# Optimization experiments

Measured on AMD Instinct MI355X. Metric: run time of the kernel, lower is better.

Reference implementation:

```python
import jax, jax.numpy as jnp
import numpy as np

B, N, DIM, HEADS = 8, 4096, 512, 8
BASE = 10000.0


def rope_cos_sin(n, dim, base=BASE):
    k_max = dim // 2
    theta = 1.0 / base ** (jnp.arange(k_max, dtype=jnp.float32) / k_max)
    angles = jnp.arange(n, dtype=jnp.float32)[:, None] * theta  # (n, k_max)
    return jnp.cos(angles), jnp.sin(angles)


def apply_rope(x, cos, sin):
    # x: (b, n, dim); complex pairs are interleaved (even=real, odd=imag)
    xr = x[..., 0::2]
    xi = x[..., 1::2]
    out_r = cos * xr - sin * xi
    out_i = sin * xr + cos * xi
    return jnp.stack([out_r, out_i], axis=-1).reshape(x.shape)


def setup_inputs() -> dict:
    key = jax.random.key(0)
    ks = jax.random.split(key, 8)
    s = 0.02
    return {
        'x': jax.random.normal(ks[0], (B, N, DIM), jnp.float32),
        'y': jax.random.normal(ks[1], (B, N, DIM), jnp.float32),
        'Wq': jax.random.normal(ks[2], (DIM, DIM), jnp.float32) * s,
        'bq': jax.random.normal(ks[3], (DIM,), jnp.float32) * s,
        'Wk': jax.random.normal(ks[4], (DIM, DIM), jnp.float32) * s,
        'bk': jax.random.normal(ks[5], (DIM,), jnp.float32) * s,
        'lepe_w': jax.random.normal(ks[6], (DIM, 1, 3), jnp.float32) * s,
        'lepe_b': jax.random.normal(ks[7], (DIM,), jnp.float32) * s,
    }


def reference(x, y, Wq, bq, Wk, bk, lepe_w, lepe_b):
    b, n, c = x.shape
    h = HEADS
    d = c // h
    q = jax.nn.elu(x @ Wq.T + bq) + 1.0
    k = jax.nn.elu(y @ Wk.T + bk) + 1.0
    cos, sin = rope_cos_sin(n, c)
    q_rope = apply_rope(q, cos, sin).reshape(b, n, h, d).transpose(0, 2, 1, 3)
    k_rope = apply_rope(k, cos, sin).reshape(b, n, h, d).transpose(0, 2, 1, 3)
    qh = q.reshape(b, n, h, d).transpose(0, 2, 1, 3)
    kh = k.reshape(b, n, h, d).transpose(0, 2, 1, 3)
    v = y.reshape(b, n, h, d).transpose(0, 2, 1, 3)
    kmean = kh.mean(axis=2, keepdims=True)  # (b,h,1,d)
    z = 1.0 / (jnp.einsum('bhnd,bhmd->bhnm', qh, kmean) + 1e-6)  # (b,h,n,1)
    scale = n ** (-0.5)
    kv = jnp.einsum('bhnd,bhne->bhde', k_rope * scale, v * scale)  # (b,h,d,d)
    out = jnp.einsum('bhnd,bhde->bhne', q_rope, kv) * z  # (b,h,n,d)
    out = out.transpose(0, 2, 1, 3).reshape(b, n, c)
    # LePE: depthwise conv1d over value stream
    vc = v.transpose(0, 2, 1, 3).reshape(b, n, c).transpose(0, 2, 1)  # (b,c,n)
    lepe = jax.lax.conv_general_dilated(
        vc, lepe_w, window_strides=(1,), padding=[(1, 1)],
        dimension_numbers=('NCH', 'OIH', 'NCH'), feature_group_count=c)
    lepe = lepe + lepe_b[None, :, None]
    return out + lepe.transpose(0, 2, 1)
```

## Files before the change

### kernel.cpp

```cpp
#include <hip/hip_runtime.h>

#define B_ 8
#define N_ 4096
#define C_ 512
#define H_ 8

typedef _Float16 h8  __attribute__((ext_vector_type(8)));
typedef _Float16 h4v __attribute__((ext_vector_type(4)));
typedef float    f4  __attribute__((ext_vector_type(4)));

static const size_t OFF_COS  = 0;
static const size_t OFF_SIN  = (size_t)4*1024*1024;
static const size_t OFF_KRH  = (size_t)8*1024*1024;
static const size_t OFF_YH   = (size_t)40*1024*1024;
static const size_t OFF_WQH  = (size_t)72*1024*1024;
static const size_t OFF_WKH  = (size_t)72*1024*1024 + 512*1024;
static const size_t OFF_KSUM = (size_t)73*1024*1024;
static const size_t OFF_KVG  = (size_t)73*1024*1024 + 64*1024;
static const size_t OFF_KVT  = (size_t)74*1024*1024 + 64*1024;

__device__ __forceinline__ unsigned int pack2h(float a, float b){
    union { _Float16 h[2]; unsigned int u; } x;
    x.h[0] = (_Float16)a; x.h[1] = (_Float16)b; return x.u;
}

__global__ void k_tables(float* __restrict__ cosT, float* __restrict__ sinT){
    int n = blockIdx.x, j = threadIdx.x;
    double th = exp((double)j * -0.035977892078031970);
    float ang = (float)n * (float)th;
    float s, c; sincosf(ang, &s, &c);
    cosT[n*256 + j] = c; sinT[n*256 + j] = s;
}

__global__ __launch_bounds__(256) void k_prep_y(
    const float* __restrict__ y, const float* __restrict__ Wq, const float* __restrict__ Wk,
    _Float16* __restrict__ yh, _Float16* __restrict__ Wqh, _Float16* __restrict__ Wkh)
{
    int bid = blockIdx.x;
    const float* src; _Float16* dst; size_t base;
    if (bid < 8192)      { src = y;  dst = yh;  base = (size_t)bid*2048; }
    else if (bid < 8320) { src = Wq; dst = Wqh; base = (size_t)(bid-8192)*2048; }
    else                 { src = Wk; dst = Wkh; base = (size_t)(bid-8320)*2048; }
    size_t o = base + (size_t)threadIdx.x*8;
    float4 a = *(const float4*)&src[o];
    float4 b = *(const float4*)&src[o+4];
    uint4 r; r.x = pack2h(a.x,a.y); r.y = pack2h(a.z,a.w); r.z = pack2h(b.x,b.y); r.w = pack2h(b.z,b.w);
    *(uint4*)&dst[o] = r;
}

__global__ __launch_bounds__(256) void k_prep_x(const float* __restrict__ x, _Float16* __restrict__ xh){
    size_t o = (size_t)blockIdx.x*2048 + (size_t)threadIdx.x*8;
    float4 a = *(const float4*)&x[o];
    float4 b = *(const float4*)&x[o+4];
    uint4 r; r.x = pack2h(a.x,a.y); r.y = pack2h(a.z,a.w); r.z = pack2h(b.x,b.y); r.w = pack2h(b.z,b.w);
    *(uint4*)&xh[o] = r;
}

__device__ __forceinline__ void stage_tile(const _Float16* __restrict__ g, _Float16* lds, int t){
#pragma unroll
    for (int i=0;i<2;++i){
        int u = i*256 + t;
        int r = u >> 2;
        int j = (u & 3) ^ ((r ^ (r >> 2)) & 3);
        __builtin_amdgcn_global_load_lds(
            (const __attribute__((address_space(1))) void*)(g + (size_t)r*C_ + j*8),
            (__attribute__((address_space(3))) void*)(lds + (size_t)(i*256 + (t & 192))*8),
            16, 0, 0);
    }
}

template<int IS_Q>
__global__ __launch_bounds__(256, IS_Q ? 3 : 4) void k_gemm(
    const _Float16* __restrict__ A, const _Float16* __restrict__ Wh, const float* __restrict__ bias,
    const float* __restrict__ cosT, const float* __restrict__ sinT,
    _Float16* __restrict__ krh, float* __restrict__ ksum,
    const float* __restrict__ ksumIn, const _Float16* __restrict__ kvTg,
    const _Float16* __restrict__ yh, const float* __restrict__ lw, const float* __restrict__ lb,
    float* __restrict__ outp)
{
    __shared__ __align__(16) char smem[IS_Q ? 53248 : 32768];
    _Float16* qrs = (_Float16*)smem;
    _Float16* kvs = (_Float16*)(smem + 36864);

    const int t = threadIdx.x;
    const int lane = t & 63;
    const int w = t >> 6;
    const int wm = w >> 1, wn = w & 1;
    const int col0 = blockIdx.x * 128;
    const int row0 = blockIdx.y * 128;
    const int lrow = lane & 15, lg = lane >> 4;
    const int b = row0 >> 12;

    if constexpr (IS_Q){
#pragma unroll
        for (int i=0;i<4;++i){
            int idx = i*256 + t;
            int hl = idx >> 9, w9 = idx & 511, e = w9 >> 3, u8 = w9 & 7;
            int j = u8 ^ (e & 7);
            int bhh = b*H_ + (col0 >> 6) + hl;
            __builtin_amdgcn_global_load_lds(
                (const __attribute__((address_space(1))) void*)(kvTg + (size_t)bhh*4096 + e*64 + j*8),
                (__attribute__((address_space(3))) void*)(kvs + (size_t)(i*256 + (t & 192))*8),
                16, 0, 0);
        }
    }

    f4 acc[4][4] = {};
    stage_tile(A  + (size_t)row0*C_, (_Float16*)(smem), t);
    stage_tile(Wh + (size_t)col0*C_, (_Float16*)(smem + 16384), t);

    const int sw = (lrow ^ (lrow >> 2)) & 3;
    const int cK = (lg ^ sw) * 8;
    int cur = 0;

    for (int kk=0; kk<16; ++kk){
        __syncthreads();
        if (kk < 15){
            stage_tile(A  + (size_t)row0*C_ + (kk+1)*32, (_Float16*)(smem + (cur^1)*8192), t);
            stage_tile(Wh + (size_t)col0*C_ + (kk+1)*32, (_Float16*)(smem + 16384 + (cur^1)*8192), t);
        }
        const _Float16* As = (const _Float16*)(smem + cur*8192);
        const _Float16* Bs = (const _Float16*)(smem + 16384 + cur*8192);
        h8 af[4], bf[4];
#pragma unroll
        for (int mi=0; mi<4; ++mi) af[mi] = *(const h8*)&As[(wm*64 + mi*16 + lrow)*32 + cK];
#pragma unroll
        for (int ni=0; ni<4; ++ni) bf[ni] = *(const h8*)&Bs[(wn*64 + ni*16 + lrow)*32 + cK];
#pragma unroll
        for (int mi=0; mi<4; ++mi)
#pragma unroll
            for (int ni=0; ni<4; ++ni)
                acc[mi][ni] = __builtin_amdgcn_mfma_f32_16x16x32_f16(af[mi], bf[ni], acc[mi][ni], 0,0,0);
        __syncthreads();
        cur ^= 1;
    }

    const int hcol0 = col0 + wn*64;
    float bcol[4], km[4];
#pragma unroll
    for (int ni=0; ni<4; ++ni){
        int c = hcol0 + ni*16 + lrow;
        bcol[ni] = bias[c];
        km[ni] = IS_Q ? ksumIn[b*C_ + c] * (1.0f/4096.0f) : 0.0f;
    }
    float colsum[4] = {0.f,0.f,0.f,0.f};
    float zr[4][4];
    _Float16* qw = qrs + w*4608;

#pragma unroll
    for (int mi=0; mi<4; ++mi){
        float qv[4][4];
#pragma unroll
        for (int ni=0; ni<4; ++ni)
#pragma unroll
            for (int r=0; r<4; ++r){
                float v = acc[mi][ni][r] + bcol[ni];
                qv[ni][r] = v > 0.f ? v + 1.f : __expf(v);
            }
        if constexpr (IS_Q){
#pragma unroll
            for (int r=0; r<4; ++r){
                float p = qv[0][r]*km[0] + qv[1][r]*km[1] + qv[2][r]*km[2] + qv[3][r]*km[3];
                p += __shfl_xor(p, 1); p += __shfl_xor(p, 2);
                p += __shfl_xor(p, 4); p += __shfl_xor(p, 8);
                zr[mi][r] = 1.0f / (p + 1e-6f);
            }
        } else {
#pragma unroll
            for (int ni=0; ni<4; ++ni)
                colsum[ni] += qv[ni][0]+qv[ni][1]+qv[ni][2]+qv[ni][3];
        }
#pragma unroll
        for (int ni=0; ni<4; ++ni){
            int c = hcol0 + ni*16 + lrow;
            int jj = c >> 1;
#pragma unroll
            for (int r=0; r<4; ++r){
                int grow = row0 + wm*64 + mi*16 + lg*4 + r;
                int n = grow & (N_-1);
                float val = qv[ni][r];
                float par = __shfl_xor(val, 1);
                float cs = cosT[n*256 + jj], sn = sinT[n*256 + jj];
                float rv = (lane & 1) ? fmaf(sn, par, cs*val) : fmaf(cs, val, -sn*par);
                float prv = __shfl_xor(rv, 1);
                if constexpr (IS_Q){
                    if (!(lane & 1))
                        *(unsigned int*)&qw[(mi*16 + lg*4 + r)*72 + (ni*16 + lrow)] = pack2h(rv, prv);
                } else {
                    if (!(lane & 1))
                        *(unsigned int*)&krh[(size_t)grow*C_ + c] = pack2h(rv, prv);
                }
            }
        }
    }

    if constexpr (!IS_Q){
#pragma unroll
        for (int ni=0; ni<4; ++ni){
            float s = colsum[ni];
            s += __shfl_xor(s, 16); s += __shfl_xor(s, 32);
            if (lane < 16) atomicAdd(&ksum[b*C_ + hcol0 + ni*16 + lane], s);
        }
    } else {
        __syncthreads();
        f4 acc2[4][4] = {};
#pragma unroll
        for (int ks=0; ks<2; ++ks){
            h8 af2[4], bf2[4];
#pragma unroll
            for (int mi2=0; mi2<4; ++mi2) af2[mi2] = *(const h8*)&qw[(mi2*16 + lrow)*72 + ks*32 + lg*8];
#pragma unroll
            for (int ni2=0; ni2<4; ++ni2){
                int e = ni2*16 + lrow;
                int du = ((ks*4 + lg) ^ (e & 7)) * 8;
                bf2[ni2] = *(const h8*)&kvs[wn*4096 + e*64 + du];
            }
#pragma unroll
            for (int mi2=0; mi2<4; ++mi2)
#pragma unroll
                for (int ni2=0; ni2<4; ++ni2)
                    acc2[mi2][ni2] = __builtin_amdgcn_mfma_f32_16x16x32_f16(af2[mi2], bf2[ni2], acc2[mi2][ni2], 0,0,0);
        }
#pragma unroll
        for (int mi2=0; mi2<4; ++mi2){
#pragma unroll
            for (int r=0; r<4; ++r){
                float z = zr[mi2][r];
#pragma unroll
                for (int ni2=0; ni2<4; ++ni2){
                    float val = acc2[mi2][ni2][r] * z;
                    float pv = __shfl_xor(val, 1);
                    if (!(lane & 1))
                        *(unsigned int*)&qw[(mi2*16 + lg*4 + r)*72 + (ni2*16 + lrow)] = pack2h(val, pv);
                }
            }
        }
        __syncthreads();
        const int cg = t & 31;
        const int c4p = cg * 4;
        const int hl = c4p >> 6;
        const int e0 = c4p & 63;
        float w0[4], w1[4], w2[4], wb[4];
#pragma unroll
        for (int j=0;j<4;++j){
            int cc = col0 + c4p + j;
            w0[j]=lw[cc*3+0]; w1[j]=lw[cc*3+1]; w2[j]=lw[cc*3+2]; wb[j]=lb[cc];
        }
#pragma unroll
        for (int i=0;i<16;++i){
            int rl = (t >> 5) + i*8;
            int grow = row0 + rl;
            int nloc = grow & (N_-1);
            int wreg = (rl >> 6)*2 + hl;
            h4v a = *(const h4v*)&qrs[wreg*4608 + (rl & 63)*72 + e0];
            const _Float16* yp = yh + (size_t)grow*C_ + col0 + c4p;
            h4v y1 = *(const h4v*)yp;
            float s0 = fmaf((float)y1[0], w1[0], wb[0]);
            float s1 = fmaf((float)y1[1], w1[1], wb[1]);
            float s2 = fmaf((float)y1[2], w1[2], wb[2]);
            float s3 = fmaf((float)y1[3], w1[3], wb[3]);
            if (nloc > 0){
                h4v y0 = *(const h4v*)(yp - C_);
                s0 = fmaf((float)y0[0], w0[0], s0); s1 = fmaf((float)y0[1], w0[1], s1);
                s2 = fmaf((float)y0[2], w0[2], s2); s3 = fmaf((float)y0[3], w0[3], s3);
            }
            if (nloc < N_-1){
                h4v y2 = *(const h4v*)(yp + C_);
                s0 = fmaf((float)y2[0], w2[0], s0); s1 = fmaf((float)y2[1], w2[1], s1);
                s2 = fmaf((float)y2[2], w2[2], s2); s3 = fmaf((float)y2[3], w2[3], s3);
            }
            float4 o;
            o.x = (float)a[0] + s0; o.y = (float)a[1] + s1;
            o.z = (float)a[2] + s2; o.w = (float)a[3] + s3;
            *(float4*)&outp[(size_t)grow*C_ + col0 + c4p] = o;
        }
    }
}

__global__ __launch_bounds__(256) void k_kv(const _Float16* __restrict__ krh, const _Float16* __restrict__ yh,
                                            float* __restrict__ kvg){
    __shared__ _Float16 krs[64*128];
    __shared__ _Float16 vs[64*128];
    const int split = blockIdx.x, bh = blockIdx.y;
    const int b = bh >> 3, h = bh & 7;
    const int t = threadIdx.x, lane = t & 63, w = t >> 6;
    const int lrow = lane & 15, lg = lane >> 4;
    f4 acc[4] = {};
    for (int sub=0; sub<4; ++sub){
        const int n0 = split*512 + sub*128;
#pragma unroll
        for (int i=0;i<8;++i){
            int q = i*256 + t;
            int d2 = q & 31, n2 = q >> 5;
            int n = n0 + 2*n2, c = h*64 + 2*d2;
            size_t g0 = (size_t)(b*N_ + n)*C_ + c;
            unsigned int u0 = *(const unsigned int*)&krh[g0];
            unsigned int u1 = *(const unsigned int*)&krh[g0 + C_];
            unsigned int v0 = *(const unsigned int*)&yh[g0];
            unsigned int v1 = *(const unsigned int*)&yh[g0 + C_];
            int chunk = n2 >> 2, j2 = (n2 & 3)*2;
            int pc0 = chunk ^ ((2*d2) & 15);
            int pc1 = pc0 ^ 1;
            *(unsigned int*)&krs[(2*d2)*128 + pc0*8 + j2]   = (u0 & 0xffffu) | (u1 << 16);
            *(unsigned int*)&krs[(2*d2+1)*128 + pc1*8 + j2] = (u0 >> 16) | (u1 & 0xffff0000u);
            *(unsigned int*)&vs[(2*d2)*128 + pc0*8 + j2]    = (v0 & 0xffffu) | (v1 << 16);
            *(unsigned int*)&vs[(2*d2+1)*128 + pc1*8 + j2]  = (v0 >> 16) | (v1 & 0xffff0000u);
        }
        __syncthreads();
#pragma unroll
        for (int ks=0; ks<4; ++ks){
            int cu = ((ks*4 + lg) ^ lrow)*8;
            h8 a = *(const h8*)&krs[(w*16 + lrow)*128 + cu];
#pragma unroll
            for (int ni=0; ni<4; ++ni){
                h8 bv = *(const h8*)&vs[(ni*16 + lrow)*128 + cu];
                acc[ni] = __builtin_amdgcn_mfma_f32_16x16x32_f16(a, bv, acc[ni], 0,0,0);
            }
        }
        __syncthreads();
    }
#pragma unroll
    for (int ni=0; ni<4; ++ni)
#pragma unroll
        for (int rr=0; rr<4; ++rr)
            atomicAdd(&kvg[(size_t)bh*4096 + (w*16 + lg*4 + rr)*64 + ni*16 + lrow],
                      acc[ni][rr] * (1.0f/4096.0f));
}

__global__ __launch_bounds__(256) void k_kvmerge(const float* __restrict__ kvg, _Float16* __restrict__ kvTg){
    int bh = blockIdx.x, t = threadIdx.x;
    const float* src = kvg + (size_t)bh*4096;
    _Float16* dst = kvTg + (size_t)bh*4096;
#pragma unroll
    for (int i=0;i<4;++i){
        int q = i*256 + t;
        int e2 = q & 31, d2 = q >> 5;
        float2 a0 = *(const float2*)&src[(2*d2)*64 + 2*e2];
        float2 a1 = *(const float2*)&src[(2*d2+1)*64 + 2*e2];
        *(unsigned int*)&dst[(2*e2)*64 + 2*d2]   = pack2h(a0.x, a1.x);
        *(unsigned int*)&dst[(2*e2+1)*64 + 2*d2] = pack2h(a0.y, a1.y);
    }
}

extern "C" void kernel_launch(void* const* d_in, const int* in_sizes, int n_in,
                              void* d_out, int out_size, void* d_ws, size_t ws_size,
                              hipStream_t stream)
{
    (void)in_sizes; (void)n_in; (void)out_size; (void)ws_size;
    const float* x  = (const float*)d_in[0];
    const float* y  = (const float*)d_in[1];
    const float* Wq = (const float*)d_in[2];
    const float* bq = (const float*)d_in[3];
    const float* Wk = (const float*)d_in[4];
    const float* bk = (const float*)d_in[5];
    const float* lw = (const float*)d_in[6];
    const float* lb = (const float*)d_in[7];

    char* ws = (char*)d_ws;
    float*    cosT = (float*)(ws + OFF_COS);
    float*    sinT = (float*)(ws + OFF_SIN);
    _Float16* krh  = (_Float16*)(ws + OFF_KRH);
    _Float16* yh   = (_Float16*)(ws + OFF_YH);
    _Float16* Wqh  = (_Float16*)(ws + OFF_WQH);
    _Float16* Wkh  = (_Float16*)(ws + OFF_WKH);
    float*    ksum = (float*)(ws + OFF_KSUM);
    float*    kvg  = (float*)(ws + OFF_KVG);
    _Float16* kvTg = (_Float16*)(ws + OFF_KVT);
    float*    out  = (float*)d_out;

    hipMemsetAsync(ws + OFF_KSUM, 0, 64*1024 + 1024*1024, stream);
    k_tables<<<dim3(N_), dim3(256), 0, stream>>>(cosT, sinT);
    k_prep_y<<<dim3(8448), dim3(256), 0, stream>>>(y, Wq, Wk, yh, Wqh, Wkh);
    k_gemm<0><<<dim3(4, 256), dim3(256), 0, stream>>>(yh, Wkh, bk, cosT, sinT,
        krh, ksum, nullptr, nullptr, nullptr, nullptr, nullptr, nullptr);
    k_kv<<<dim3(8, 64), dim3(256), 0, stream>>>(krh, yh, kvg);
    k_kvmerge<<<dim3(64), dim3(256), 0, stream>>>(kvg, kvTg);
    k_prep_x<<<dim3(8192), dim3(256), 0, stream>>>(x, krh);
    k_gemm<1><<<dim3(4, 256), dim3(256), 0, stream>>>(krh, Wqh, bq, cosT, sinT,
        nullptr, nullptr, ksum, kvTg, yh, lw, lb, out);
}
```

Baseline: 210.7 us.

## Halve GEMM row tile to 64 and load kv fragments directly into registers

The k_gemm kernels now use 64x128 output tiles instead of 128x128, with the grid doubled and LDS cut to 24 KB so more blocks fit per CU (launch bounds raised to 5). In the Q path the kv matrix is no longer staged through LDS. Each wave loads its kv MFMA B-fragments straight from global memory into registers before the second matmul. The goal is more occupancy and less LDS pressure, at the cost of reloading the W tile twice as often and repeating kv loads in every block.

```diff
diff --git a/kernel.cpp b/kernel.cpp
--- a/kernel.cpp
+++ b/kernel.cpp
@@ -56,7 +56,15 @@
     *(uint4*)&xh[o] = r;
 }
 
-__device__ __forceinline__ void stage_tile(const _Float16* __restrict__ g, _Float16* lds, int t){
+__device__ __forceinline__ void stage_a64(const _Float16* __restrict__ g, _Float16* lds, int t){
+    int r = t >> 2;
+    int j = (t & 3) ^ ((r ^ (r >> 2)) & 3);
+    __builtin_amdgcn_global_load_lds(
+        (const __attribute__((address_space(1))) void*)(g + (size_t)r*C_ + j*8),
+        (__attribute__((address_space(3))) void*)(lds + (size_t)(t & 192)*8),
+        16, 0, 0);
+}
+__device__ __forceinline__ void stage_b128(const _Float16* __restrict__ g, _Float16* lds, int t){
 #pragma unroll
     for (int i=0;i<2;++i){
         int u = i*256 + t;
@@ -70,7 +78,7 @@
 }
 
 template<int IS_Q>
-__global__ __launch_bounds__(256, IS_Q ? 3 : 4) void k_gemm(
+__global__ __launch_bounds__(256, 5) void k_gemm(
     const _Float16* __restrict__ A, const _Float16* __restrict__ Wh, const float* __restrict__ bias,
     const float* __restrict__ cosT, const float* __restrict__ sinT,
     _Float16* __restrict__ krh, float* __restrict__ ksum,
@@ -78,36 +86,21 @@
     const _Float16* __restrict__ yh, const float* __restrict__ lw, const float* __restrict__ lb,
     float* __restrict__ outp)
 {
-    __shared__ __align__(16) char smem[IS_Q ? 53248 : 32768];
+    __shared__ __align__(16) char smem[24576];
     _Float16* qrs = (_Float16*)smem;
-    _Float16* kvs = (_Float16*)(smem + 36864);
 
     const int t = threadIdx.x;
     const int lane = t & 63;
     const int w = t >> 6;
     const int wm = w >> 1, wn = w & 1;
     const int col0 = blockIdx.x * 128;
-    const int row0 = blockIdx.y * 128;
+    const int row0 = blockIdx.y * 64;
     const int lrow = lane & 15, lg = lane >> 4;
     const int b = row0 >> 12;
 
-    if constexpr (IS_Q){
-#pragma unroll
-        for (int i=0;i<4;++i){
-            int idx = i*256 + t;
-            int hl = idx >> 9, w9 = idx & 511, e = w9 >> 3, u8 = w9 & 7;
-            int j = u8 ^ (e & 7);
-            int bhh = b*H_ + (col0 >> 6) + hl;
-            __builtin_amdgcn_global_load_lds(
-                (const __attribute__((address_space(1))) void*)(kvTg + (size_t)bhh*4096 + e*64 + j*8),
-                (__attribute__((address_space(3))) void*)(kvs + (size_t)(i*256 + (t & 192))*8),
-                16, 0, 0);
-        }
-    }
-
-    f4 acc[4][4] = {};
-    stage_tile(A  + (size_t)row0*C_, (_Float16*)(smem), t);
-    stage_tile(Wh + (size_t)col0*C_, (_Float16*)(smem + 16384), t);
+    f4 acc[2][4] = {};
+    stage_a64(A  + (size_t)row0*C_, (_Float16*)smem, t);
+    stage_b128(Wh + (size_t)col0*C_, (_Float16*)(smem + 8192), t);
 
     const int sw = (lrow ^ (lrow >> 2)) & 3;
     const int cK = (lg ^ sw) * 8;
@@ -116,18 +109,18 @@
     for (int kk=0; kk<16; ++kk){
         __syncthreads();
         if (kk < 15){
-            stage_tile(A  + (size_t)row0*C_ + (kk+1)*32, (_Float16*)(smem + (cur^1)*8192), t);
-            stage_tile(Wh + (size_t)col0*C_ + (kk+1)*32, (_Float16*)(smem + 16384 + (cur^1)*8192), t);
-        }
-        const _Float16* As = (const _Float16*)(smem + cur*8192);
-        const _Float16* Bs = (const _Float16*)(smem + 16384 + cur*8192);
-        h8 af[4], bf[4];
-#pragma unroll
-        for (int mi=0; mi<4; ++mi) af[mi] = *(const h8*)&As[(wm*64 + mi*16 + lrow)*32 + cK];
+            stage_a64(A  + (size_t)row0*C_ + (kk+1)*32, (_Float16*)(smem + (cur^1)*4096), t);
+            stage_b128(Wh + (size_t)col0*C_ + (kk+1)*32, (_Float16*)(smem + 8192 + (cur^1)*8192), t);
+        }
+        const _Float16* As = (const _Float16*)(smem + cur*4096);
+        const _Float16* Bs = (const _Float16*)(smem + 8192 + cur*8192);
+        h8 af[2], bf[4];
+#pragma unroll
+        for (int mi=0; mi<2; ++mi) af[mi] = *(const h8*)&As[(wm*32 + mi*16 + lrow)*32 + cK];
 #pragma unroll
         for (int ni=0; ni<4; ++ni) bf[ni] = *(const h8*)&Bs[(wn*64 + ni*16 + lrow)*32 + cK];
 #pragma unroll
-        for (int mi=0; mi<4; ++mi)
+        for (int mi=0; mi<2; ++mi)
 #pragma unroll
             for (int ni=0; ni<4; ++ni)
                 acc[mi][ni] = __builtin_amdgcn_mfma_f32_16x16x32_f16(af[mi], bf[ni], acc[mi][ni], 0,0,0);
@@ -144,11 +137,11 @@
         km[ni] = IS_Q ? ksumIn[b*C_ + c] * (1.0f/4096.0f) : 0.0f;
     }
     float colsum[4] = {0.f,0.f,0.f,0.f};
-    float zr[4][4];
-    _Float16* qw = qrs + w*4608;
-
-#pragma unroll
-    for (int mi=0; mi<4; ++mi){
+    float zr[2][4];
+    _Float16* qw = qrs + w*2304;
+
+#pragma unroll
+    for (int mi=0; mi<2; ++mi){
         float qv[4][4];
 #pragma unroll
         for (int ni=0; ni<4; ++ni)
@@ -176,7 +169,7 @@
             int jj = c >> 1;
 #pragma unroll
             for (int r=0; r<4; ++r){
-                int grow = row0 + wm*64 + mi*16 + lg*4 + r;
+                int grow = row0 + wm*32 + mi*16 + lg*4 + r;
                 int n = grow & (N_-1);
                 float val = qv[ni][r];
                 float par = __shfl_xor(val, 1);
@@ -202,27 +195,28 @@
             if (lane < 16) atomicAdd(&ksum[b*C_ + hcol0 + ni*16 + lane], s);
         }
     } else {
-        __syncthreads();
-        f4 acc2[4][4] = {};
-#pragma unroll
-        for (int ks=0; ks<2; ++ks){
-            h8 af2[4], bf2[4];
-#pragma unroll
-            for (int mi2=0; mi2<4; ++mi2) af2[mi2] = *(const h8*)&qw[(mi2*16 + lrow)*72 + ks*32 + lg*8];
+        const int bhh = b*H_ + (col0 >> 6) + wn;
+        h8 kv0[4], kv1[4];
+#pragma unroll
+        for (int ni2=0; ni2<4; ++ni2){
+            int e = ni2*16 + lrow;
+            kv0[ni2] = *(const h8*)&kvTg[(size_t)bhh*4096 + e*64 + lg*8];
+            kv1[ni2] = *(const h8*)&kvTg[(size_t)bhh*4096 + e*64 + 32 + lg*8];
+        }
+        __syncthreads();
+        f4 acc2[2][4] = {};
+#pragma unroll
+        for (int mi2=0; mi2<2; ++mi2){
+            h8 a0 = *(const h8*)&qw[(mi2*16 + lrow)*72 + 0*32 + lg*8];
+            h8 a1 = *(const h8*)&qw[(mi2*16 + lrow)*72 + 1*32 + lg*8];
 #pragma unroll
             for (int ni2=0; ni2<4; ++ni2){
-                int e = ni2*16 + lrow;
-                int du = ((ks*4 + lg) ^ (e & 7)) * 8;
-                bf2[ni2] = *(const h8*)&kvs[wn*4096 + e*64 + du];
-            }
-#pragma unroll
-            for (int mi2=0; mi2<4; ++mi2)
-#pragma unroll
-                for (int ni2=0; ni2<4; ++ni2)
-                    acc2[mi2][ni2] = __builtin_amdgcn_mfma_f32_16x16x32_f16(af2[mi2], bf2[ni2], acc2[mi2][ni2], 0,0,0);
-        }
-#pragma unroll
-        for (int mi2=0; mi2<4; ++mi2){
+                acc2[mi2][ni2] = __builtin_amdgcn_mfma_f32_16x16x32_f16(a0, kv0[ni2], acc2[mi2][ni2], 0,0,0);
+                acc2[mi2][ni2] = __builtin_amdgcn_mfma_f32_16x16x32_f16(a1, kv1[ni2], acc2[mi2][ni2], 0,0,0);
+            }
+        }
+#pragma unroll
+        for (int mi2=0; mi2<2; ++mi2){
 #pragma unroll
             for (int r=0; r<4; ++r){
                 float z = zr[mi2][r];
@@ -247,12 +241,12 @@
             w0[j]=lw[cc*3+0]; w1[j]=lw[cc*3+1]; w2[j]=lw[cc*3+2]; wb[j]=lb[cc];
         }
 #pragma unroll
-        for (int i=0;i<16;++i){
+        for (int i=0;i<8;++i){
             int rl = (t >> 5) + i*8;
             int grow = row0 + rl;
             int nloc = grow & (N_-1);
-            int wreg = (rl >> 6)*2 + hl;
-            h4v a = *(const h4v*)&qrs[wreg*4608 + (rl & 63)*72 + e0];
+            int wreg = ((rl >> 5) << 1) + hl;
+            h4v a = *(const h4v*)&qrs[wreg*2304 + (rl & 31)*72 + e0];
             const _Float16* yp = yh + (size_t)grow*C_ + col0 + c4p;
             h4v y1 = *(const h4v*)yp;
             float s0 = fmaf((float)y1[0], w1[0], wb[0]);
@@ -371,11 +365,11 @@
     hipMemsetAsync(ws + OFF_KSUM, 0, 64*1024 + 1024*1024, stream);
     k_tables<<<dim3(N_), dim3(256), 0, stream>>>(cosT, sinT);
     k_prep_y<<<dim3(8448), dim3(256), 0, stream>>>(y, Wq, Wk, yh, Wqh, Wkh);
-    k_gemm<0><<<dim3(4, 256), dim3(256), 0, stream>>>(yh, Wkh, bk, cosT, sinT,
+    k_gemm<0><<<dim3(4, 512), dim3(256), 0, stream>>>(yh, Wkh, bk, cosT, sinT,
         krh, ksum, nullptr, nullptr, nullptr, nullptr, nullptr, nullptr);
     k_kv<<<dim3(8, 64), dim3(256), 0, stream>>>(krh, yh, kvg);
     k_kvmerge<<<dim3(64), dim3(256), 0, stream>>>(kvg, kvTg);
     k_prep_x<<<dim3(8192), dim3(256), 0, stream>>>(x, krh);
-    k_gemm<1><<<dim3(4, 256), dim3(256), 0, stream>>>(krh, Wqh, bq, cosT, sinT,
+    k_gemm<1><<<dim3(4, 512), dim3(256), 0, stream>>>(krh, Wqh, bq, cosT, sinT,
         nullptr, nullptr, ksum, kvTg, yh, lw, lb, out);
 }
```

New measurement: 200.5 us. 4.8% less time.
